# Optimization experiments

Measured on AMD Instinct MI355X. Metric: run time of the kernel, lower is better.

## Reference

```python
import jax, jax.numpy as jnp
import numpy as np

D, N, K = 6, 32768, 16          # depths, nodes per depth, max children
V, DIN, DOUT = 100000, 64, 64   # vocab, embed dim, hidden dim


def setup_inputs() -> dict:
    key = jax.random.key(0)
    ks = jax.random.split(key, 6)
    labels = jax.random.randint(ks[0], (D, N), 0, V, dtype=jnp.int32)
    # child index 0 == no child (masked); 1..N index previous depth's nodes
    child_idx = jax.random.randint(ks[1], (D, N, K), 0, N + 1, dtype=jnp.int32)
    E = jax.random.uniform(ks[2], (V, DIN), jnp.float32, -0.05, 0.05)
    s_in = 1.0 / np.sqrt(DIN)
    W_w = jax.random.uniform(ks[3], (DIN, 4 * DOUT), jnp.float32, -s_in, s_in)
    W_b = jnp.zeros((4 * DOUT,), jnp.float32)
    s_out = 1.0 / np.sqrt(DOUT)
    U_f = jax.random.uniform(ks[4], (DOUT, DOUT), jnp.float32, -s_out, s_out)
    U_iuo = jax.random.uniform(ks[5], (DOUT, 3 * DOUT), jnp.float32, -s_out, s_out)
    return {"labels": labels, "child_idx": child_idx, "E": E,
            "W_w": W_w, "W_b": W_b, "U_f": U_f, "U_iuo": U_iuo}


def _tree_lstm(labels, child_idx, E, W_w, W_b, U_f, U_iuo):
    d = U_f.shape[0]
    n = labels.shape[1]
    zero_row = jnp.zeros((1, d), jnp.float32)

    def step(carry, inp):
        h_prev, c_prev = carry            # [N+1, d], row 0 = zero init state
        lab, idx = inp                    # [N], [N, K]
        x = E[lab]                        # [N, din] embedding lookup
        mask = (idx != 0).astype(jnp.float32)   # [N, K]
        h = h_prev[idx]                   # [N, K, d] gather children hidden
        c = c_prev[idx]                   # [N, K, d] gather children cell
        h_sum = jnp.einsum('nkd,nk->nd', h, mask)  # masked child-sum
        Wx = x @ W_w + W_b                # [N, 4d]
        W_f_x, W_i_x, W_u_x, W_o_x = jnp.split(Wx, 4, axis=-1)
        # per-child forget gate
        f_k = jax.nn.sigmoid(W_f_x[:, None, :] + jnp.einsum('nkd,de->nke', h, U_f))
        branch_f = jnp.einsum('nkd,nkd,nk->nd', f_k, c, mask)
        iuo = h_sum @ U_iuo               # [N, 3d]
        i_g = jax.nn.sigmoid(iuo[:, :d] + W_i_x)
        u_g = jnp.tanh(iuo[:, d:2 * d] + W_u_x)
        o_g = jax.nn.sigmoid(iuo[:, 2 * d:] + W_o_x)
        new_c = i_g * u_g + branch_f
        new_h = o_g * jnp.tanh(new_c)
        h_next = jnp.concatenate([zero_row, new_h], 0)
        c_next = jnp.concatenate([zero_row, new_c], 0)
        return (h_next, c_next), None

    init = (jnp.zeros((n + 1, d), jnp.float32), jnp.zeros((n + 1, d), jnp.float32))
    (h_fin, _c_fin), _ = jax.lax.scan(step, init, (labels, child_idx))
    return h_fin[1:]                      # final-depth (roots) hidden [N, d]


def reference(labels, child_idx, E, W_w, W_b, U_f, U_iuo):
    return _tree_lstm(labels, child_idx, E, W_w, W_b, U_f, U_iuo)
```

## Files before the change

kernel.cpp:

```cpp
#include <hip/hip_runtime.h>

#define NN 32768
#define KK 16
#define DD 6

typedef short short8 __attribute__((ext_vector_type(8)));
typedef float floatx4 __attribute__((ext_vector_type(4)));

__device__ __forceinline__ float sigm(float x) { return 1.0f / (1.0f + __expf(-x)); }
__device__ __forceinline__ float ftanh(float x) {
    float e = __expf(2.0f * x);
    return 1.0f - 2.0f / (e + 1.0f);
}
__device__ __forceinline__ unsigned short f2bf(float x) {
    union { float f; unsigned u; } v; v.f = x;
    unsigned r = v.u + 0x7FFF + ((v.u >> 16) & 1);
    return (unsigned short)(r >> 16);
}
__device__ __forceinline__ float bf2f(unsigned short h) {
    union { unsigned u; float f; } v; v.u = ((unsigned)h) << 16; return v.f;
}

__global__ __launch_bounds__(256) void k0_all(
    const int* __restrict__ labels, const float* __restrict__ E,
    const float* __restrict__ W_w, const float* __restrict__ W_b,
    _Float16* __restrict__ WxAll)
{
    __shared__ int labs[64];
    __shared__ __align__(16) unsigned short Ax[64][74];
    __shared__ __align__(16) unsigned short Bw[256][74];
    const int tid = threadIdx.x;
    const int blk = blockIdx.x & 511;
    const int dep = blockIdx.x >> 9;
    const int n0 = blk * 64;
    _Float16* __restrict__ Wx = WxAll + (size_t)dep * NN * 256;
    if (tid < 64) labs[tid] = labels[(size_t)dep * NN + n0 + tid];
    __syncthreads();
    {
        const int m = tid >> 2, q = tid & 3;
        const float4* e4 = (const float4*)(E + (size_t)labs[m] * 64 + q * 16);
#pragma unroll
        for (int i = 0; i < 4; ++i) {
            float4 v = e4[i];
            Ax[m][q * 16 + i * 4 + 0] = f2bf(v.x);
            Ax[m][q * 16 + i * 4 + 1] = f2bf(v.y);
            Ax[m][q * 16 + i * 4 + 2] = f2bf(v.z);
            Ax[m][q * 16 + i * 4 + 3] = f2bf(v.w);
        }
    }
    {
        const int c = tid;
#pragma unroll 4
        for (int k = 0; k < 64; ++k) Bw[c][k] = f2bf(W_w[k * 256 + c]);
    }
    __syncthreads();
    const int ln = tid & 63, wv = tid >> 6;
    const int lr = ln & 15, qd = ln >> 4;
    short8 af[2];
#pragma unroll
    for (int ks = 0; ks < 2; ++ks)
        af[ks] = *(const short8*)&Ax[wv * 16 + lr][ks * 32 + qd * 8];
    floatx4 acc[16];
#pragma unroll
    for (int nt = 0; nt < 16; ++nt) acc[nt] = (floatx4){0.f, 0.f, 0.f, 0.f};
#pragma unroll
    for (int nt = 0; nt < 16; ++nt) {
#pragma unroll
        for (int ks = 0; ks < 2; ++ks) {
            short8 bw = *(const short8*)&Bw[nt * 16 + lr][ks * 32 + qd * 8];
            acc[nt] = __builtin_amdgcn_mfma_f32_16x16x32_bf16(af[ks], bw, acc[nt], 0, 0, 0);
        }
    }
#pragma unroll
    for (int nt = 0; nt < 16; ++nt) {
        const int col = nt * 16 + lr;
        const float bb = W_b[col];
#pragma unroll
        for (int r = 0; r < 4; ++r) {
            const int node = n0 + wv * 16 + qd * 4 + r;
            Wx[(size_t)node * 256 + col] = (_Float16)(acc[nt][r] + bb);
        }
    }
}

__global__ __launch_bounds__(256) void kd_fused(
    const int* __restrict__ cidx, const uint2* __restrict__ sprev,
    const _Float16* __restrict__ Wx, const float* __restrict__ U_iuo,
    const float* __restrict__ U_f, uint2* __restrict__ snext,
    float* __restrict__ out, int first, int last)
{
    __shared__ __align__(16) unsigned short Bi[192][68];
    __shared__ __align__(16) unsigned short Bf[64][68];
    __shared__ __align__(16) unsigned short Ah[64][68];
    __shared__ __align__(16) unsigned short AlHs[64][68];
    const int tid = threadIdx.x;
    const int n0 = blockIdx.x * 64;
    if (tid < 192) {
        const int c = tid;
#pragma unroll 4
        for (int k = 0; k < 64; ++k) Bi[c][k] = f2bf(U_iuo[k * 192 + c]);
    } else {
        const int c = tid - 192;
#pragma unroll 4
        for (int k = 0; k < 64; ++k) Bf[c][k] = f2bf(U_f[k * 64 + c]);
    }
    const int ln = tid & 63, wv = tid >> 6;
    const int lr = ln & 15, qd = ln >> 4;

    float hs[4][4] = {{0.f}}, bfv[4][4] = {{0.f}};
    if (!first) {
        float wfx[4][4];
#pragma unroll
        for (int r = 0; r < 4; ++r)
#pragma unroll
            for (int nt = 0; nt < 4; ++nt)
                wfx[r][nt] = (float)Wx[(size_t)(n0 + wv * 16 + qd * 4 + r) * 256
                                       + nt * 16 + lr];
#pragma unroll 1
        for (int k = 0; k < KK; ++k) {
            int id[4];
#pragma unroll
            for (int r = 0; r < 4; ++r)
                id[r] = cidx[(size_t)(n0 + wv * 16 + qd * 4 + r) * KK + k];
            uint2 v[4][4];
#pragma unroll
            for (int r = 0; r < 4; ++r)
#pragma unroll
                for (int nt = 0; nt < 4; ++nt)
                    v[r][nt] = sprev[(size_t)id[r] * 64 + nt * 16 + lr];
#pragma unroll
            for (int r = 0; r < 4; ++r)
#pragma unroll
                for (int nt = 0; nt < 4; ++nt) {
                    const float h = (float)(short)(v[r][nt].x & 0xFFFFu) * (1.f / 32767.f);
                    const float g = (float)((int)v[r][nt].x >> 16) * (1.f / 2048.f);
                    const float c = __uint_as_float(v[r][nt].y);
                    hs[r][nt] += h;
                    bfv[r][nt] = fmaf(sigm(wfx[r][nt] + g), c, bfv[r][nt]);
                }
        }
    }
#pragma unroll
    for (int r = 0; r < 4; ++r)
#pragma unroll
        for (int nt = 0; nt < 4; ++nt) {
            const int m = wv * 16 + qd * 4 + r, col = nt * 16 + lr;
            const unsigned short hi = f2bf(hs[r][nt]);
            Ah[m][col] = hi;
            AlHs[m][col] = f2bf(hs[r][nt] - bf2f(hi));
        }
    __syncthreads();
    short8 ah[2], al[2];
#pragma unroll
    for (int ks = 0; ks < 2; ++ks) {
        ah[ks] = *(const short8*)&Ah[wv * 16 + lr][ks * 32 + qd * 8];
        al[ks] = *(const short8*)&AlHs[wv * 16 + lr][ks * 32 + qd * 8];
    }
    floatx4 acc[12];
#pragma unroll
    for (int nt = 0; nt < 12; ++nt) {
        floatx4 a = (floatx4){0.f, 0.f, 0.f, 0.f};
#pragma unroll
        for (int ks = 0; ks < 2; ++ks) {
            const short8 bu = *(const short8*)&Bi[nt * 16 + lr][ks * 32 + qd * 8];
            a = __builtin_amdgcn_mfma_f32_16x16x32_bf16(al[ks], bu, a, 0, 0, 0);
            a = __builtin_amdgcn_mfma_f32_16x16x32_bf16(ah[ks], bu, a, 0, 0, 0);
        }
        acc[nt] = a;
    }
    float nhv[4][4], ncv[4][4];
#pragma unroll
    for (int nt = 0; nt < 4; ++nt) {
        const int col = nt * 16 + lr;
#pragma unroll
        for (int r = 0; r < 4; ++r) {
            const int node = n0 + wv * 16 + qd * 4 + r;
            const _Float16* __restrict__ wxr = Wx + (size_t)node * 256;
            const float ig = sigm(acc[nt][r] + (float)wxr[64 + col]);
            const float ug = ftanh(acc[4 + nt][r] + (float)wxr[128 + col]);
            const float og = sigm(acc[8 + nt][r] + (float)wxr[192 + col]);
            const float nc = fmaf(ig, ug, bfv[r][nt]);
            const float nh = og * ftanh(nc);
            nhv[nt][r] = nh;
            ncv[nt][r] = nc;
            if (last) {
                out[(size_t)node * 64 + col] = nh;
            } else {
                AlHs[wv * 16 + qd * 4 + r][col] = f2bf(nh);
            }
        }
    }
    if (!last) {
        short8 ag[2];
#pragma unroll
        for (int ks = 0; ks < 2; ++ks)
            ag[ks] = *(const short8*)&AlHs[wv * 16 + lr][ks * 32 + qd * 8];
        floatx4 g[4];
#pragma unroll
        for (int nt = 0; nt < 4; ++nt) {
            g[nt] = (floatx4){0.f, 0.f, 0.f, 0.f};
#pragma unroll
            for (int ks = 0; ks < 2; ++ks) {
                const short8 bfr = *(const short8*)&Bf[nt * 16 + lr][ks * 32 + qd * 8];
                g[nt] = __builtin_amdgcn_mfma_f32_16x16x32_bf16(ag[ks], bfr, g[nt], 0, 0, 0);
            }
        }
#pragma unroll
        for (int nt = 0; nt < 4; ++nt) {
#pragma unroll
            for (int r = 0; r < 4; ++r) {
                const int node = n0 + wv * 16 + qd * 4 + r;
                const int hq = (int)rintf(nhv[nt][r] * 32767.f);
                const int gq = (int)rintf(g[nt][r] * 2048.f);
                uint2 pw;
                pw.x = ((unsigned)hq & 0xFFFFu) | ((unsigned)gq << 16);
                pw.y = __float_as_uint(ncv[nt][r]);
                snext[(size_t)(node + 1) * 64 + nt * 16 + lr] = pw;
            }
        }
        if (blockIdx.x == 0 && tid < 64)
            snext[tid] = make_uint2(0u, 0u);
    }
}

extern "C" void kernel_launch(void* const* d_in, const int* in_sizes, int n_in,
                              void* d_out, int out_size, void* d_ws, size_t ws_size,
                              hipStream_t stream)
{
    const int*   labels = (const int*)d_in[0];
    const int*   child  = (const int*)d_in[1];
    const float* E      = (const float*)d_in[2];
    const float* W_w    = (const float*)d_in[3];
    const float* W_b    = (const float*)d_in[4];
    const float* U_f    = (const float*)d_in[5];
    const float* U_iuo  = (const float*)d_in[6];
    float* out = (float*)d_out;

    uint2* s0 = (uint2*)d_ws;
    uint2* s1 = s0 + (size_t)(NN + 1) * 64;
    _Float16* WxAll = (_Float16*)(s1 + (size_t)(NN + 1) * 64);

    k0_all<<<6 * (NN / 64), 256, 0, stream>>>(labels, E, W_w, W_b, WxAll);

    uint2* sp = s0;
    uint2* sn = s1;
    for (int d = 0; d < DD; ++d) {
        const int last = (d == DD - 1);
        kd_fused<<<NN / 64, 256, 0, stream>>>(
            child + (size_t)d * NN * KK, sp, WxAll + (size_t)d * NN * 256,
            U_iuo, U_f, sn, out, d == 0, last);
        uint2* ts = sp; sp = sn; sn = ts;
    }
}
```

Before: 366.3 us.

## Overlap next-depth Wx projection with current depth and double-buffer child gathers

Replaces the upfront all-depth Wx projection kernel with one that computes only depth 0, then merges the next depth's projection into each depth kernel as extra blocks (1024-block grid) so it runs alongside the gather-heavy recurrence. The child gather loop is also software-pipelined with two register buffers, prefetching child indices and state rows for the next child while the current one is consumed. The aim is to hide gather latency and fill idle CUs. In exchange it raises register pressure, and the merged kernel's larger shared LDS footprint may reduce occupancy.

After: 431.3 us. +17.7%, slower.

```diff
diff --git a/kernel.cpp b/kernel.cpp
--- a/kernel.cpp
+++ b/kernel.cpp
@@ -21,20 +21,17 @@
     union { unsigned u; float f; } v; v.u = ((unsigned)h) << 16; return v.f;
 }
 
-__global__ __launch_bounds__(256) void k0_all(
+__device__ __forceinline__ void wx_role(
     const int* __restrict__ labels, const float* __restrict__ E,
     const float* __restrict__ W_w, const float* __restrict__ W_b,
-    _Float16* __restrict__ WxAll)
-{
-    __shared__ int labs[64];
-    __shared__ __align__(16) unsigned short Ax[64][74];
-    __shared__ __align__(16) unsigned short Bw[256][74];
+    _Float16* __restrict__ Wx, int blk, unsigned short* lds)
+{
+    unsigned short (*Ax)[74] = (unsigned short(*)[74])lds;
+    unsigned short (*Bw)[74] = (unsigned short(*)[74])(lds + 64 * 74);
+    int* labs = (int*)(lds + 320 * 74);
     const int tid = threadIdx.x;
-    const int blk = blockIdx.x & 511;
-    const int dep = blockIdx.x >> 9;
     const int n0 = blk * 64;
-    _Float16* __restrict__ Wx = WxAll + (size_t)dep * NN * 256;
-    if (tid < 64) labs[tid] = labels[(size_t)dep * NN + n0 + tid];
+    if (tid < 64) labs[tid] = labels[n0 + tid];
     __syncthreads();
     {
         const int m = tid >> 2, q = tid & 3;
@@ -83,16 +80,32 @@
     }
 }
 
-__global__ __launch_bounds__(256) void kd_fused(
-    const int* __restrict__ cidx, const uint2* __restrict__ sprev,
-    const _Float16* __restrict__ Wx, const float* __restrict__ U_iuo,
-    const float* __restrict__ U_f, uint2* __restrict__ snext,
-    float* __restrict__ out, int first, int last)
-{
-    __shared__ __align__(16) unsigned short Bi[192][68];
-    __shared__ __align__(16) unsigned short Bf[64][68];
-    __shared__ __align__(16) unsigned short Ah[64][68];
-    __shared__ __align__(16) unsigned short AlHs[64][68];
+__global__ __launch_bounds__(256) void k0_one(
+    const int* __restrict__ labels, const float* __restrict__ E,
+    const float* __restrict__ W_w, const float* __restrict__ W_b,
+    _Float16* __restrict__ Wx)
+{
+    __shared__ __align__(16) unsigned short lds[23808];
+    wx_role(labels, E, W_w, W_b, Wx, blockIdx.x, lds);
+}
+
+__global__ __launch_bounds__(256) void kd_merged(
+    const int* __restrict__ labels_next, const int* __restrict__ cidx,
+    const uint2* __restrict__ sprev, const _Float16* __restrict__ Wx,
+    _Float16* __restrict__ WxNext, const float* __restrict__ E,
+    const float* __restrict__ W_w, const float* __restrict__ W_b,
+    const float* __restrict__ U_iuo, const float* __restrict__ U_f,
+    uint2* __restrict__ snext, float* __restrict__ out, int first, int last)
+{
+    __shared__ __align__(16) unsigned short LDS[26112];
+    if (blockIdx.x >= 512) {
+        wx_role(labels_next, E, W_w, W_b, WxNext, blockIdx.x - 512, LDS);
+        return;
+    }
+    unsigned short (*Bi)[68]   = (unsigned short(*)[68])LDS;
+    unsigned short (*Bf)[68]   = (unsigned short(*)[68])(LDS + 192*68);
+    unsigned short (*Ah)[68]   = (unsigned short(*)[68])(LDS + 256*68);
+    unsigned short (*AlHs)[68] = (unsigned short(*)[68])(LDS + 320*68);
     const int tid = threadIdx.x;
     const int n0 = blockIdx.x * 64;
     if (tid < 192) {
@@ -116,18 +129,20 @@
             for (int nt = 0; nt < 4; ++nt)
                 wfx[r][nt] = (float)Wx[(size_t)(n0 + wv * 16 + qd * 4 + r) * 256
                                        + nt * 16 + lr];
-#pragma unroll 1
-        for (int k = 0; k < KK; ++k) {
-            int id[4];
-#pragma unroll
-            for (int r = 0; r < 4; ++r)
-                id[r] = cidx[(size_t)(n0 + wv * 16 + qd * 4 + r) * KK + k];
-            uint2 v[4][4];
-#pragma unroll
-            for (int r = 0; r < 4; ++r)
-#pragma unroll
-                for (int nt = 0; nt < 4; ++nt)
-                    v[r][nt] = sprev[(size_t)id[r] * 64 + nt * 16 + lr];
+        const size_t cb = (size_t)(n0 + wv * 16 + qd * 4) * KK;
+        int ida[4], idb[4];
+        uint2 va[4][4], vb[4][4];
+#pragma unroll
+        for (int r = 0; r < 4; ++r) ida[r] = cidx[cb + r * KK];
+#pragma unroll
+        for (int r = 0; r < 4; ++r)
+#pragma unroll
+            for (int nt = 0; nt < 4; ++nt)
+                va[r][nt] = sprev[(size_t)ida[r] * 64 + nt * 16 + lr];
+#pragma unroll
+        for (int r = 0; r < 4; ++r) idb[r] = cidx[cb + r * KK + 1];
+
+        auto consume = [&](uint2 (&v)[4][4]) {
 #pragma unroll
             for (int r = 0; r < 4; ++r)
 #pragma unroll
@@ -138,6 +153,31 @@
                     hs[r][nt] += h;
                     bfv[r][nt] = fmaf(sigm(wfx[r][nt] + g), c, bfv[r][nt]);
                 }
+        };
+#pragma unroll 1
+        for (int k = 0; k < KK; k += 2) {
+#pragma unroll
+            for (int r = 0; r < 4; ++r)
+#pragma unroll
+                for (int nt = 0; nt < 4; ++nt)
+                    vb[r][nt] = sprev[(size_t)idb[r] * 64 + nt * 16 + lr];
+            if (k + 2 < KK) {
+#pragma unroll
+                for (int r = 0; r < 4; ++r) ida[r] = cidx[cb + r * KK + k + 2];
+            }
+            consume(va);
+            if (k + 2 < KK) {
+#pragma unroll
+                for (int r = 0; r < 4; ++r)
+#pragma unroll
+                    for (int nt = 0; nt < 4; ++nt)
+                        va[r][nt] = sprev[(size_t)ida[r] * 64 + nt * 16 + lr];
+            }
+            if (k + 3 < KK) {
+#pragma unroll
+                for (int r = 0; r < 4; ++r) idb[r] = cidx[cb + r * KK + k + 3];
+            }
+            consume(vb);
         }
     }
 #pragma unroll
@@ -240,15 +280,19 @@
     uint2* s1 = s0 + (size_t)(NN + 1) * 64;
     _Float16* WxAll = (_Float16*)(s1 + (size_t)(NN + 1) * 64);
 
-    k0_all<<<6 * (NN / 64), 256, 0, stream>>>(labels, E, W_w, W_b, WxAll);
+    k0_one<<<512, 256, 0, stream>>>(labels, E, W_w, W_b, WxAll);
 
     uint2* sp = s0;
     uint2* sn = s1;
     for (int d = 0; d < DD; ++d) {
         const int last = (d == DD - 1);
-        kd_fused<<<NN / 64, 256, 0, stream>>>(
-            child + (size_t)d * NN * KK, sp, WxAll + (size_t)d * NN * 256,
-            U_iuo, U_f, sn, out, d == 0, last);
+        const int grid = last ? 512 : 1024;
+        kd_merged<<<grid, 256, 0, stream>>>(
+            labels + (size_t)(last ? d : d + 1) * NN,
+            child + (size_t)d * NN * KK, sp,
+            WxAll + (size_t)d * NN * 256,
+            WxAll + (size_t)(last ? d : d + 1) * NN * 256,
+            E, W_w, W_b, U_iuo, U_f, sn, out, d == 0, last);
         uint2* ts = sp; sp = sn; sn = ts;
     }
 }
```

## Store Wx in MFMA-fragment layout and double-buffer child state gathers

Applied to the files above, without the earlier changes.

The precomputed Wx projection is now written and read in a per-wave fragment-native layout, so each lane does one 8-byte half4 store or load per tile instead of four scattered 2-byte accesses. The child-gather loop in the depth kernel is software-pipelined with two register buffers, so the gathers and index loads for the next child are issued before the current child is processed. This is meant to cut uncoalesced Wx traffic and hide gather latency, at the cost of more registers and possibly lower occupancy.

Result: no change. 363.4 us (-0.8%).

```diff
diff --git a/kernel.cpp b/kernel.cpp
--- a/kernel.cpp
+++ b/kernel.cpp
@@ -6,6 +6,7 @@
 
 typedef short short8 __attribute__((ext_vector_type(8)));
 typedef float floatx4 __attribute__((ext_vector_type(4)));
+typedef _Float16 half4v __attribute__((ext_vector_type(4)));
 
 __device__ __forceinline__ float sigm(float x) { return 1.0f / (1.0f + __expf(-x)); }
 __device__ __forceinline__ float ftanh(float x) {
@@ -24,7 +25,7 @@
 __global__ __launch_bounds__(256) void k0_all(
     const int* __restrict__ labels, const float* __restrict__ E,
     const float* __restrict__ W_w, const float* __restrict__ W_b,
-    _Float16* __restrict__ WxAll)
+    _Float16* __restrict__ WxF)
 {
     __shared__ int labs[64];
     __shared__ __align__(16) unsigned short Ax[64][74];
@@ -33,7 +34,6 @@
     const int blk = blockIdx.x & 511;
     const int dep = blockIdx.x >> 9;
     const int n0 = blk * 64;
-    _Float16* __restrict__ Wx = WxAll + (size_t)dep * NN * 256;
     if (tid < 64) labs[tid] = labels[(size_t)dep * NN + n0 + tid];
     __syncthreads();
     {
@@ -71,15 +71,15 @@
             acc[nt] = __builtin_amdgcn_mfma_f32_16x16x32_bf16(af[ks], bw, acc[nt], 0, 0, 0);
         }
     }
+    _Float16* __restrict__ base =
+        WxF + ((size_t)(dep * 512 + blk) * 4 + wv) * 16 * 256 + (size_t)ln * 4;
 #pragma unroll
     for (int nt = 0; nt < 16; ++nt) {
-        const int col = nt * 16 + lr;
-        const float bb = W_b[col];
-#pragma unroll
-        for (int r = 0; r < 4; ++r) {
-            const int node = n0 + wv * 16 + qd * 4 + r;
-            Wx[(size_t)node * 256 + col] = (_Float16)(acc[nt][r] + bb);
-        }
+        const float bb = W_b[nt * 16 + lr];
+        half4v hv;
+#pragma unroll
+        for (int r = 0; r < 4; ++r) hv[r] = (_Float16)(acc[nt][r] + bb);
+        *(half4v*)&base[nt * 256] = hv;
     }
 }
 
@@ -106,28 +106,32 @@
     }
     const int ln = tid & 63, wv = tid >> 6;
     const int lr = ln & 15, qd = ln >> 4;
+    const _Float16* __restrict__ wbase =
+        Wx + ((size_t)blockIdx.x * 4 + wv) * 16 * 256 + (size_t)ln * 4;
 
     float hs[4][4] = {{0.f}}, bfv[4][4] = {{0.f}};
     if (!first) {
         float wfx[4][4];
 #pragma unroll
+        for (int nt = 0; nt < 4; ++nt) {
+            const half4v fv = *(const half4v*)&wbase[nt * 256];
+#pragma unroll
+            for (int r = 0; r < 4; ++r) wfx[r][nt] = (float)fv[r];
+        }
+        const size_t cb = (size_t)(n0 + wv * 16 + qd * 4) * KK;
+        int ida[4], idb[4];
+        uint2 va[4][4], vb[4][4];
+#pragma unroll
+        for (int r = 0; r < 4; ++r) ida[r] = cidx[cb + r * KK];
+#pragma unroll
         for (int r = 0; r < 4; ++r)
 #pragma unroll
             for (int nt = 0; nt < 4; ++nt)
-                wfx[r][nt] = (float)Wx[(size_t)(n0 + wv * 16 + qd * 4 + r) * 256
-                                       + nt * 16 + lr];
-#pragma unroll 1
-        for (int k = 0; k < KK; ++k) {
-            int id[4];
-#pragma unroll
-            for (int r = 0; r < 4; ++r)
-                id[r] = cidx[(size_t)(n0 + wv * 16 + qd * 4 + r) * KK + k];
-            uint2 v[4][4];
-#pragma unroll
-            for (int r = 0; r < 4; ++r)
-#pragma unroll
-                for (int nt = 0; nt < 4; ++nt)
-                    v[r][nt] = sprev[(size_t)id[r] * 64 + nt * 16 + lr];
+                va[r][nt] = sprev[(size_t)ida[r] * 64 + nt * 16 + lr];
+#pragma unroll
+        for (int r = 0; r < 4; ++r) idb[r] = cidx[cb + r * KK + 1];
+
+        auto consume = [&](uint2 (&v)[4][4]) {
 #pragma unroll
             for (int r = 0; r < 4; ++r)
 #pragma unroll
@@ -138,6 +142,31 @@
                     hs[r][nt] += h;
                     bfv[r][nt] = fmaf(sigm(wfx[r][nt] + g), c, bfv[r][nt]);
                 }
+        };
+#pragma unroll 1
+        for (int k = 0; k < KK; k += 2) {
+#pragma unroll
+            for (int r = 0; r < 4; ++r)
+#pragma unroll
+                for (int nt = 0; nt < 4; ++nt)
+                    vb[r][nt] = sprev[(size_t)idb[r] * 64 + nt * 16 + lr];
+            if (k + 2 < KK) {
+#pragma unroll
+                for (int r = 0; r < 4; ++r) ida[r] = cidx[cb + r * KK + k + 2];
+            }
+            consume(va);
+            if (k + 2 < KK) {
+#pragma unroll
+                for (int r = 0; r < 4; ++r)
+#pragma unroll
+                    for (int nt = 0; nt < 4; ++nt)
+                        va[r][nt] = sprev[(size_t)ida[r] * 64 + nt * 16 + lr];
+            }
+            if (k + 3 < KK) {
+#pragma unroll
+                for (int r = 0; r < 4; ++r) idb[r] = cidx[cb + r * KK + k + 3];
+            }
+            consume(vb);
         }
     }
 #pragma unroll
@@ -172,13 +201,15 @@
 #pragma unroll
     for (int nt = 0; nt < 4; ++nt) {
         const int col = nt * 16 + lr;
+        const half4v iv = *(const half4v*)&wbase[(4 + nt) * 256];
+        const half4v uv = *(const half4v*)&wbase[(8 + nt) * 256];
+        const half4v ov = *(const half4v*)&wbase[(12 + nt) * 256];
 #pragma unroll
         for (int r = 0; r < 4; ++r) {
             const int node = n0 + wv * 16 + qd * 4 + r;
-            const _Float16* __restrict__ wxr = Wx + (size_t)node * 256;
-            const float ig = sigm(acc[nt][r] + (float)wxr[64 + col]);
-            const float ug = ftanh(acc[4 + nt][r] + (float)wxr[128 + col]);
-            const float og = sigm(acc[8 + nt][r] + (float)wxr[192 + col]);
+            const float ig = sigm(acc[nt][r] + (float)iv[r]);
+            const float ug = ftanh(acc[4 + nt][r] + (float)uv[r]);
+            const float og = sigm(acc[8 + nt][r] + (float)ov[r]);
             const float nc = fmaf(ig, ug, bfv[r][nt]);
             const float nh = og * ftanh(nc);
             nhv[nt][r] = nh;
@@ -238,16 +269,17 @@
 
     uint2* s0 = (uint2*)d_ws;
     uint2* s1 = s0 + (size_t)(NN + 1) * 64;
-    _Float16* WxAll = (_Float16*)(s1 + (size_t)(NN + 1) * 64);
-
-    k0_all<<<6 * (NN / 64), 256, 0, stream>>>(labels, E, W_w, W_b, WxAll);
+    _Float16* WxF = (_Float16*)(s1 + (size_t)(NN + 1) * 64);
+
+    k0_all<<<6 * (NN / 64), 256, 0, stream>>>(labels, E, W_w, W_b, WxF);
 
     uint2* sp = s0;
     uint2* sn = s1;
     for (int d = 0; d < DD; ++d) {
         const int last = (d == DD - 1);
         kd_fused<<<NN / 64, 256, 0, stream>>>(
-            child + (size_t)d * NN * KK, sp, WxAll + (size_t)d * NN * 256,
+            child + (size_t)d * NN * KK, sp,
+            WxF + (size_t)d * NN * 256,
             U_iuo, U_f, sn, out, d == 0, last);
         uint2* ts = sp; sp = sn; sn = ts;
     }
```
